# Optimization experiments

Hardware: AMD Instinct MI355X
Metric: run time of the kernel (lower is better)

Reference implementation:

```python
import jax, jax.numpy as jnp
import numpy as np

N = 32768
E = 262144
OUT = 512
H = 8
DH = OUT // H


def setup_inputs() -> dict:
    key = jax.random.key(0)
    ks = jax.random.split(key, 12)
    s = 0.02
    return {
        "h": jax.random.normal(ks[0], (N, 512), dtype=jnp.float32),
        "row": jax.random.randint(ks[1], (E,), 0, N, dtype=jnp.int32),
        "col": jax.random.randint(ks[2], (E,), 0, N, dtype=jnp.int32),
        "W_in": jax.random.normal(ks[3], (512, OUT), dtype=jnp.float32) * s,
        "b_in": jnp.zeros((OUT,), dtype=jnp.float32),
        "W_q": jax.random.normal(ks[4], (OUT, OUT), dtype=jnp.float32) * s,
        "b_q": jnp.zeros((OUT,), dtype=jnp.float32),
        "W_k": jax.random.normal(ks[5], (OUT, OUT), dtype=jnp.float32) * s,
        "b_k": jnp.zeros((OUT,), dtype=jnp.float32),
        "W_v": jax.random.normal(ks[6], (OUT, OUT), dtype=jnp.float32) * s,
        "b_v": jnp.zeros((OUT,), dtype=jnp.float32),
    }


def reference(h, row, col, W_in, b_in, W_q, b_q, W_k, b_k, W_v, b_v):
    scaling = DH ** -0.5
    x = h @ W_in + b_in                                   # [N, OUT]
    q = ((x @ W_q + b_q) * scaling).reshape(N, H, DH)     # [N, H, DH]
    k = (x @ W_k + b_k).reshape(N, H, DH)
    v = (x @ W_v + b_v).reshape(N, H, DH)

    # bsddmm: per-edge, per-head attention logits only at adjacency nonzeros
    logits = jnp.einsum("ehd,ehd->eh", q[row], k[col])    # [E, H]

    # sparse row-wise softmax over each node's incident edges
    m = jax.ops.segment_max(logits, row, num_segments=N)  # [N, H]
    ex = jnp.exp(logits - m[row])                         # [E, H]
    denom = jax.ops.segment_sum(ex, row, num_segments=N)  # [N, H]
    attn = ex / denom[row]                                # [E, H]

    # bspmm: aggregate v over neighbors with sparse attention weights
    out = jax.ops.segment_sum(attn[:, :, None] * v[col], row, num_segments=N)  # [N, H, DH]
    return out
```

## Files before the change

kernel.cpp:

```cpp
#include <hip/hip_runtime.h>

#define NN 32768
#define EE 262144
#define DM 512
#define NQKV 1536
#define NHEAD 8
#define DHEAD 64

typedef unsigned short u16;
typedef unsigned int u32;
typedef __attribute__((ext_vector_type(8))) short bf16x8;
typedef __attribute__((ext_vector_type(4))) float f32x4;
typedef __attribute__((ext_vector_type(8))) u16 u16x8;
typedef __attribute__((ext_vector_type(4))) u32 u32x4;

__device__ __forceinline__ float bf2f(u16 u) {
  union { u32 i; float f; } x; x.i = ((u32)u) << 16; return x.f;
}
__device__ __forceinline__ float bflo(u32 p) {
  union { u32 i; float f; } x; x.i = p << 16; return x.f;
}
__device__ __forceinline__ float bfhi(u32 p) {
  union { u32 i; float f; } x; x.i = p & 0xFFFF0000u; return x.f;
}
__device__ __forceinline__ u16 f2bf(float f) {
  union { float f; u32 i; } x; x.f = f;
  u32 r = x.i + 0x7FFFu + ((x.i >> 16) & 1u);
  return (u16)(r >> 16);
}

__device__ __forceinline__ void load_lds16(const u16* g, u16* l) {
  __builtin_amdgcn_global_load_lds(
      (const __attribute__((address_space(1))) char*)(const void*)g,
      (__attribute__((address_space(3))) char*)(void*)l, 16, 0, 0);
}

__device__ __forceinline__ int swz(int r, int s) {
  return s ^ (r & 3) ^ ((r >> 2) & 1);
}

#define GB_CASTH 8192
#define GB_CASTW 128
#define GB_CNTD  1024
#define GB_TCW   192
#define GB_BIAS  96
__global__ void prep_all(const float* __restrict__ h, u16* __restrict__ hb,
                         const float* __restrict__ Win, u16* __restrict__ Winb,
                         const int* __restrict__ row, int* __restrict__ deg,
                         const float* __restrict__ Wq, const float* __restrict__ Wk,
                         const float* __restrict__ Wv, u16* __restrict__ At,
                         const float* __restrict__ bin, const float* __restrict__ bq,
                         const float* __restrict__ bk, const float* __restrict__ bv,
                         float* __restrict__ bias) {
  __shared__ float t[64][65];
  const int tid = threadIdx.x;
  int b = blockIdx.x;

  if (b < GB_CASTH) {
    const int i = (b * 256 + tid) * 8;
    float4 a = *(const float4*)&h[i];
    float4 c = *(const float4*)&h[i + 4];
    u16x8 o = { f2bf(a.x), f2bf(a.y), f2bf(a.z), f2bf(a.w),
                f2bf(c.x), f2bf(c.y), f2bf(c.z), f2bf(c.w) };
    *(u16x8*)&hb[i] = o;
    return;
  }
  b -= GB_CASTH;
  if (b < GB_CASTW) {
    const int i = (b * 256 + tid) * 8;
    float4 a = *(const float4*)&Win[i];
    float4 c = *(const float4*)&Win[i + 4];
    u16x8 o = { f2bf(a.x), f2bf(a.y), f2bf(a.z), f2bf(a.w),
                f2bf(c.x), f2bf(c.y), f2bf(c.z), f2bf(c.w) };
    *(u16x8*)&Winb[i] = o;
    return;
  }
  b -= GB_CASTW;
  if (b < GB_CNTD) {
    const int e = b * 256 + tid;
    atomicAdd(&deg[row[e]], 1);
    return;
  }
  b -= GB_CNTD;
  if (b < GB_TCW) {
    const int z = b / 64;
    const int r64 = b % 64;
    const float* W = (z == 0) ? Wq : (z == 1) ? Wk : Wv;
    const float scale = (z == 0) ? 0.125f : 1.0f;
    const int m0 = (r64 >> 3) * 64;
    const int j0 = (r64 & 7) * 64;
    const int tx = tid & 63, ty = tid >> 6;
#pragma unroll
    for (int i = 0; i < 16; ++i) {
      const int r = ty * 16 + i;
      t[r][tx] = W[(size_t)(m0 + r) * 512 + (j0 + tx)];
    }
    __syncthreads();
#pragma unroll
    for (int i = 0; i < 16; ++i) {
      const int j = j0 + ty * 16 + i;
      const int pr = (z == 0) ? j : (512 + 2 * j + (z - 1));
      At[(size_t)pr * 512 + (m0 + tx)] = f2bf(t[tx][ty * 16 + i] * scale);
    }
    return;
  }
  b -= GB_TCW;
  {
    const int j = (b % 6) * 256 + tid;
    const int m0 = (b / 6) * 32;
    const float* Wsel; const float* bsel; int jj; float scale = 1.0f; int pos;
    if (j < 512)       { Wsel = Wq; bsel = bq; jj = j;        scale = 0.125f; pos = j; }
    else if (j < 1024) { Wsel = Wk; bsel = bk; jj = j - 512;  pos = 512 + 2 * jj; }
    else               { Wsel = Wv; bsel = bv; jj = j - 1024; pos = 513 + 2 * jj; }
    float s0 = 0.f, s1 = 0.f, s2 = 0.f, s3 = 0.f;
#pragma unroll
    for (int m = 0; m < 32; m += 4) {
      s0 = fmaf(bin[m0 + m],     Wsel[(size_t)(m0 + m)     * 512 + jj], s0);
      s1 = fmaf(bin[m0 + m + 1], Wsel[(size_t)(m0 + m + 1) * 512 + jj], s1);
      s2 = fmaf(bin[m0 + m + 2], Wsel[(size_t)(m0 + m + 2) * 512 + jj], s2);
      s3 = fmaf(bin[m0 + m + 3], Wsel[(size_t)(m0 + m + 3) * 512 + jj], s3);
    }
    float add = ((s0 + s1) + (s2 + s3)) * scale;
    if (m0 == 0) add += bsel[jj] * scale;
    atomicAdd(&bias[pos], add);
  }
}

__global__ void scan_deg(const int* __restrict__ deg, int* __restrict__ row_ptr,
                         int* __restrict__ cursor) {
  __shared__ int sums[1024];
  const int t = threadIdx.x;
  const int base = t * 32;
  int loc[32];
  int s = 0;
#pragma unroll
  for (int i = 0; i < 32; ++i) { loc[i] = s; s += deg[base + i]; }
  sums[t] = s;
  __syncthreads();
  for (int off = 1; off < 1024; off <<= 1) {
    int v = (t >= off) ? sums[t - off] : 0;
    __syncthreads();
    sums[t] += v;
    __syncthreads();
  }
  const int excl = sums[t] - s;
#pragma unroll
  for (int i = 0; i < 32; ++i) {
    const int val = excl + loc[i];
    row_ptr[base + i] = val;
    cursor[base + i] = val;
  }
  if (t == 1023) row_ptr[NN] = sums[1023];
}

__global__ void fill_csr(const int* __restrict__ row, const int* __restrict__ col,
                         int* __restrict__ cursor, int* __restrict__ dst) {
  const int e = blockIdx.x * 256 + threadIdx.x;
  const int r = row[e];
  const int p = atomicAdd(&cursor[r], 1);
  dst[p] = col[e];
}

__global__ __launch_bounds__(256, 2) void gemm_wt(
    const u16* __restrict__ A,
    const u16* __restrict__ B,
    u16* __restrict__ C) {
  __shared__ u16 As[2][128 * 32];
  __shared__ u16 Bs[2][128 * 32];
  const int tid = threadIdx.x;
  const int lane = tid & 63;
  const int wave = tid >> 6;
  const int quad = lane >> 4;
  const int l16 = lane & 15;
  const int m0 = blockIdx.y * 128;
  const int n0 = blockIdx.x * 128;
  const int wm = (wave >> 1) * 64;
  const int wn = (wave & 1) * 64;

  const int c0 = tid, c1 = tid + 256;
  const int r0 = c0 >> 2, ko0 = swz(r0, c0 & 3) * 8;
  const int r1 = c1 >> 2, ko1 = swz(r1, c1 & 3) * 8;
  const u16* Ag0 = A + (size_t)(m0 + r0) * DM + ko0;
  const u16* Ag1 = A + (size_t)(m0 + r1) * DM + ko1;
  const u16* Bg0 = B + (size_t)(n0 + r0) * DM + ko0;
  const u16* Bg1 = B + (size_t)(n0 + r1) * DM + ko1;

  f32x4 acc[4][4];
#pragma unroll
  for (int i = 0; i < 4; ++i)
#pragma unroll
    for (int j = 0; j < 4; ++j) acc[i][j] = (f32x4){0.f, 0.f, 0.f, 0.f};

  load_lds16(Ag0, &As[0][c0 * 8]);
  load_lds16(Bg0, &Bs[0][c0 * 8]);
  load_lds16(Ag1, &As[0][c1 * 8]);
  load_lds16(Bg1, &Bs[0][c1 * 8]);
  __syncthreads();

  int cur = 0;
#pragma unroll
  for (int kt = 32; kt < DM; kt += 32) {
    load_lds16(Ag0 + kt, &As[cur ^ 1][c0 * 8]);
    load_lds16(Bg0 + kt, &Bs[cur ^ 1][c0 * 8]);
    load_lds16(Ag1 + kt, &As[cur ^ 1][c1 * 8]);
    load_lds16(Bg1 + kt, &Bs[cur ^ 1][c1 * 8]);
    bf16x8 a[4], b[4];
#pragma unroll
    for (int i = 0; i < 4; ++i) {
      const int ra = wm + i * 16 + l16;
      const int rb = wn + i * 16 + l16;
      a[i] = *(const bf16x8*)&As[cur][ra * 32 + swz(ra, quad) * 8];
      b[i] = *(const bf16x8*)&Bs[cur][rb * 32 + swz(rb, quad) * 8];
    }
#pragma unroll
    for (int mi = 0; mi < 4; ++mi)
#pragma unroll
      for (int ni = 0; ni < 4; ++ni)
        acc[mi][ni] = __builtin_amdgcn_mfma_f32_16x16x32_bf16(a[mi], b[ni], acc[mi][ni], 0, 0, 0);
    __syncthreads();
    cur ^= 1;
  }
  {
    bf16x8 a[4], b[4];
#pragma unroll
    for (int i = 0; i < 4; ++i) {
      const int ra = wm + i * 16 + l16;
      const int rb = wn + i * 16 + l16;
      a[i] = *(const bf16x8*)&As[cur][ra * 32 + swz(ra, quad) * 8];
      b[i] = *(const bf16x8*)&Bs[cur][rb * 32 + swz(rb, quad) * 8];
    }
#pragma unroll
    for (int mi = 0; mi < 4; ++mi)
#pragma unroll
      for (int ni = 0; ni < 4; ++ni)
        acc[mi][ni] = __builtin_amdgcn_mfma_f32_16x16x32_bf16(a[mi], b[ni], acc[mi][ni], 0, 0, 0);
  }

#pragma unroll
  for (int ni = 0; ni < 4; ++ni) {
    const int coln = n0 + wn + ni * 16 + l16;
#pragma unroll
    for (int mi = 0; mi < 4; ++mi) {
#pragma unroll
      for (int r = 0; r < 4; ++r) {
        const int rowm = m0 + wm + mi * 16 + quad * 4 + r;
        C[(size_t)rowm * 512 + coln] = f2bf(acc[mi][ni][r]);
      }
    }
  }
}

__global__ __launch_bounds__(256, 2) void gemm_qkv(
    const u16* __restrict__ A,
    const u16* __restrict__ B,
    const float* __restrict__ bias,
    u16* __restrict__ C) {
  __shared__ u16 As[3][128 * 32];
  __shared__ u16 Bs[3][128 * 32];
  const int tid = threadIdx.x;
  const int lane = tid & 63;
  const int wave = tid >> 6;
  const int quad = lane >> 4;
  const int l16 = lane & 15;

  const int bid = blockIdx.y * 12 + blockIdx.x;
  const int sw = (bid & 7) * 384 + (bid >> 3);
  const int bx = sw % 12;
  const int by = sw / 12;
  const int m0 = by * 128;
  const int n0 = bx * 128;
  const int wm = (wave >> 1) * 64;
  const int wn = (wave & 1) * 64;

  const int c0 = tid, c1 = tid + 256;
  const int r0 = c0 >> 2, ko0 = swz(r0, c0 & 3) * 8;
  const int r1 = c1 >> 2, ko1 = swz(r1, c1 & 3) * 8;
  const u16* Ag0 = A + (size_t)(m0 + r0) * DM + ko0;
  const u16* Ag1 = A + (size_t)(m0 + r1) * DM + ko1;
  const u16* Bg0 = B + (size_t)(n0 + r0) * DM + ko0;
  const u16* Bg1 = B + (size_t)(n0 + r1) * DM + ko1;

  f32x4 acc[4][4];
#pragma unroll
  for (int i = 0; i < 4; ++i)
#pragma unroll
    for (int j = 0; j < 4; ++j) acc[i][j] = (f32x4){0.f, 0.f, 0.f, 0.f};

  load_lds16(Ag0, &As[0][c0 * 8]);
  load_lds16(Bg0, &Bs[0][c0 * 8]);
  load_lds16(Ag1, &As[0][c1 * 8]);
  load_lds16(Bg1, &Bs[0][c1 * 8]);
  load_lds16(Ag0 + 32, &As[1][c0 * 8]);
  load_lds16(Bg0 + 32, &Bs[1][c0 * 8]);
  load_lds16(Ag1 + 32, &As[1][c1 * 8]);
  load_lds16(Bg1 + 32, &Bs[1][c1 * 8]);

#pragma unroll
  for (int t = 0; t < 16; ++t) {
    const int bt = t % 3;
    if (t < 15) asm volatile("s_waitcnt vmcnt(4) lgkmcnt(0)\n\ts_barrier" ::: "memory");
    else        asm volatile("s_waitcnt vmcnt(0) lgkmcnt(0)\n\ts_barrier" ::: "memory");
    if (t < 14) {
      const int b2 = (t + 2) % 3;
      const int kg = (t + 2) * 32;
      load_lds16(Ag0 + kg, &As[b2][c0 * 8]);
      load_lds16(Bg0 + kg, &Bs[b2][c0 * 8]);
      load_lds16(Ag1 + kg, &As[b2][c1 * 8]);
      load_lds16(Bg1 + kg, &Bs[b2][c1 * 8]);
    }
    bf16x8 a[4], b[4];
#pragma unroll
    for (int i = 0; i < 4; ++i) {
      const int ra = wm + i * 16 + l16;
      const int rb = wn + i * 16 + l16;
      a[i] = *(const bf16x8*)&As[bt][ra * 32 + swz(ra, quad) * 8];
      b[i] = *(const bf16x8*)&Bs[bt][rb * 32 + swz(rb, quad) * 8];
    }
#pragma unroll
    for (int mi = 0; mi < 4; ++mi)
#pragma unroll
      for (int ni = 0; ni < 4; ++ni)
        acc[mi][ni] = __builtin_amdgcn_mfma_f32_16x16x32_bf16(a[mi], b[ni], acc[mi][ni], 0, 0, 0);
  }

#pragma unroll
  for (int ni = 0; ni < 4; ++ni) {
    const int coln = n0 + wn + ni * 16 + l16;
    const float bv = bias[coln];
#pragma unroll
    for (int mi = 0; mi < 4; ++mi) {
#pragma unroll
      for (int r = 0; r < 4; ++r) {
        const int rowm = m0 + wm + mi * 16 + quad * 4 + r;
        C[(size_t)rowm * NQKV + coln] = f2bf(acc[mi][ni][r] + bv);
      }
    }
  }
}

__global__ __launch_bounds__(256) void attn_agg(
    const u16* __restrict__ qkv16, const u32* __restrict__ qkv32,
    const int* __restrict__ row_ptr, const int* __restrict__ dst,
    float* __restrict__ out) {
  const int gt = blockIdx.x * 256 + threadIdx.x;
  const int node = gt >> 6;
  const int lane = gt & 63;
  const u16x8 qr = *(const u16x8*)&qkv16[(size_t)node * NQKV + lane * 8];
  float qf[8];
#pragma unroll
  for (int j = 0; j < 8; ++j) qf[j] = bf2f(qr[j]);

  const int beg = row_ptr[node];
  const int end = row_ptr[node + 1];
  float acc[8] = {0.f,0.f,0.f,0.f,0.f,0.f,0.f,0.f};
  float denom = 0.f;

  for (int e = beg; e < end; e += 4) {
    u32 p[4][8];
    int idx[4];
#pragma unroll
    for (int jj = 0; jj < 4; ++jj) {
      const int ee = min(e + jj, end - 1);
      idx[jj] = dst[ee];
    }
#pragma unroll
    for (int jj = 0; jj < 4; ++jj) {
      const u32* pp = qkv32 + (size_t)idx[jj] * 768 + 256 + lane * 8;
      *(u32x4*)&p[jj][0] = *(const u32x4*)pp;
      *(u32x4*)&p[jj][4] = *(const u32x4*)(pp + 4);
    }
#pragma unroll
    for (int jj = 0; jj < 4; ++jj) {
      float s = 0.f;
#pragma unroll
      for (int j = 0; j < 8; ++j) s = fmaf(qf[j], bflo(p[jj][j]), s);
      s += __shfl_xor(s, 1, 64);
      s += __shfl_xor(s, 2, 64);
      s += __shfl_xor(s, 4, 64);
      const float ex = (e + jj < end) ? __expf(s) : 0.f;
      denom += ex;
#pragma unroll
      for (int j = 0; j < 8; ++j) acc[j] = fmaf(ex, bfhi(p[jj][j]), acc[j]);
    }
  }

  const float inv = (end > beg) ? (1.0f / denom) : 0.f;
  float4 o0 = { acc[0] * inv, acc[1] * inv, acc[2] * inv, acc[3] * inv };
  float4 o1 = { acc[4] * inv, acc[5] * inv, acc[6] * inv, acc[7] * inv };
  float* op = &out[(size_t)node * 512 + lane * 8];
  *(float4*)op = o0;
  *(float4*)(op + 4) = o1;
}

extern "C" void kernel_launch(void* const* d_in, const int* in_sizes, int n_in,
                              void* d_out, int out_size, void* d_ws, size_t ws_size,
                              hipStream_t stream) {
  const float* h   = (const float*)d_in[0];
  const int*   row = (const int*)d_in[1];
  const int*   col = (const int*)d_in[2];
  const float* Win = (const float*)d_in[3];
  const float* bin = (const float*)d_in[4];
  const float* Wq  = (const float*)d_in[5];
  const float* bq  = (const float*)d_in[6];
  const float* Wk  = (const float*)d_in[7];
  const float* bk  = (const float*)d_in[8];
  const float* Wv  = (const float*)d_in[9];
  const float* bv  = (const float*)d_in[10];
  float* out = (float*)d_out;

  char* ws = (char*)d_ws;
  u16*   qkv     = (u16*)(ws + 0);
  u16*   hb      = (u16*)(ws + 100663296);
  u16*   Wt      = (u16*)(ws + 134217728);
  float* bias    = (float*)(ws + 135790592);
  int*   deg     = (int*)(ws + 135796736);
  int*   row_ptr = (int*)(ws + 135927808);
  int*   cursor  = (int*)(ws + 136058888);
  int*   dst     = (int*)(ws + 136189960);
  u16*   At      = (u16*)(ws + 0);
  u16*   Winb    = (u16*)(ws + 1572864);

  (void)hipMemsetAsync(deg, 0, NN * sizeof(int), stream);
  (void)hipMemsetAsync(bias, 0, NQKV * sizeof(float), stream);
  hipLaunchKernelGGL(prep_all,
                     dim3(GB_CASTH + GB_CASTW + GB_CNTD + GB_TCW + GB_BIAS),
                     dim3(256), 0, stream,
                     h, hb, Win, Winb, row, deg, Wq, Wk, Wv, At,
                     bin, bq, bk, bv, bias);
  hipLaunchKernelGGL(scan_deg,  dim3(1), dim3(1024), 0, stream, deg, row_ptr, cursor);
  hipLaunchKernelGGL(fill_csr,  dim3(EE / 256), dim3(256), 0, stream, row, col, cursor, dst);
  hipLaunchKernelGGL(gemm_wt,   dim3(512 / 128, 1536 / 128), dim3(256), 0, stream, At, Winb, Wt);
  hipLaunchKernelGGL(gemm_qkv,  dim3(NQKV / 128, NN / 128), dim3(256), 0, stream, hb, Wt, bias, qkv);
  hipLaunchKernelGGL(attn_agg,  dim3((NN * 64) / 256), dim3(256), 0, stream,
                     qkv, (const u32*)qkv, row_ptr, dst, out);
}
```

Measured before the change: 338.8 us.

## Fold weight-product GEMM into prep kernel using fp32 SIMT tiles

Removes the separate transposed-weight cast and bf16 MFMA gemm_wt launch. The prep kernel now directly computes the combined (W_q|W_k|W_v)^T·W_in^T product in fp32 with shared-memory tiled FMAs, placing these long blocks first in the grid. Bias folding now uses one block per column group over all 512 rows with no atomics, which also drops the bias memset. This saves one kernel launch plus the intermediate casts, but does the 1536x512x512 weight product on SIMT lanes instead of matrix cores, so those 192 blocks may become a long tail.

```diff
diff --git a/kernel.cpp b/kernel.cpp
--- a/kernel.cpp
+++ b/kernel.cpp
@@ -39,90 +39,101 @@
   return s ^ (r & 3) ^ ((r >> 2) & 1);
 }
 
+#define GB_WT    192
+#define GB_BIAS  6
+#define GB_CNTD  1024
 #define GB_CASTH 8192
-#define GB_CASTW 128
-#define GB_CNTD  1024
-#define GB_TCW   192
-#define GB_BIAS  96
-__global__ void prep_all(const float* __restrict__ h, u16* __restrict__ hb,
-                         const float* __restrict__ Win, u16* __restrict__ Winb,
-                         const int* __restrict__ row, int* __restrict__ deg,
-                         const float* __restrict__ Wq, const float* __restrict__ Wk,
-                         const float* __restrict__ Wv, u16* __restrict__ At,
-                         const float* __restrict__ bin, const float* __restrict__ bq,
-                         const float* __restrict__ bk, const float* __restrict__ bv,
-                         float* __restrict__ bias) {
-  __shared__ float t[64][65];
+__global__ __launch_bounds__(256) void prep_mega(
+    const float* __restrict__ h, u16* __restrict__ hb,
+    const float* __restrict__ Win,
+    const float* __restrict__ Wq, const float* __restrict__ Wk,
+    const float* __restrict__ Wv, u16* __restrict__ Wt,
+    const float* __restrict__ bin, const float* __restrict__ bq,
+    const float* __restrict__ bk, const float* __restrict__ bv,
+    float* __restrict__ bias,
+    const int* __restrict__ row, int* __restrict__ deg) {
+  __shared__ float As[32][68];
+  __shared__ float Bs[64][36];
   const int tid = threadIdx.x;
   int b = blockIdx.x;
 
-  if (b < GB_CASTH) {
+  if (b < GB_WT) {
+    const int jt = b >> 3;
+    const int kt = b & 7;
+    const int z = jt >> 3;
+    const float* W = (z == 0) ? Wq : (z == 1) ? Wk : Wv;
+    const float scale = (z == 0) ? 0.125f : 1.0f;
+    const int jj0 = (jt & 7) * 64;
+    const int kk0 = kt * 64;
+    const int tj = tid >> 4, tk = tid & 15;
+    float acc[4][4] = {};
+    for (int k0 = 0; k0 < 512; k0 += 32) {
+#pragma unroll
+      for (int i = 0; i < 8; ++i) {
+        const int idx = tid + i * 256;
+        const int ami = idx >> 6, ajo = idx & 63;
+        As[ami][ajo] = W[(size_t)(k0 + ami) * 512 + jj0 + ajo];
+        const int bkk = idx >> 5, bmi = idx & 31;
+        Bs[bkk][bmi] = Win[(size_t)(kk0 + bkk) * 512 + k0 + bmi];
+      }
+      __syncthreads();
+#pragma unroll
+      for (int mi = 0; mi < 32; ++mi) {
+        float4 av = *(const float4*)&As[mi][tj * 4];
+        const float* ap = (const float*)&av;
+        float bv4[4] = { Bs[tk * 4 + 0][mi], Bs[tk * 4 + 1][mi],
+                         Bs[tk * 4 + 2][mi], Bs[tk * 4 + 3][mi] };
+#pragma unroll
+        for (int a2 = 0; a2 < 4; ++a2)
+#pragma unroll
+          for (int b2 = 0; b2 < 4; ++b2)
+            acc[a2][b2] = fmaf(ap[a2], bv4[b2], acc[a2][b2]);
+      }
+      __syncthreads();
+    }
+#pragma unroll
+    for (int a2 = 0; a2 < 4; ++a2) {
+      const int j = jt * 64 + tj * 4 + a2;
+      const int pr = (j < 512) ? j
+                   : (j < 1024) ? (512 + 2 * (j - 512))
+                                : (513 + 2 * (j - 1024));
+#pragma unroll
+      for (int b2 = 0; b2 < 4; ++b2)
+        Wt[(size_t)pr * 512 + kk0 + tk * 4 + b2] = f2bf(acc[a2][b2] * scale);
+    }
+    return;
+  }
+  b -= GB_WT;
+  if (b < GB_BIAS) {
+    const int j = b * 256 + tid;
+    const float* Wsel; const float* bsel; int jj; float scale = 1.0f; int pos;
+    if (j < 512)       { Wsel = Wq; bsel = bq; jj = j;        scale = 0.125f; pos = j; }
+    else if (j < 1024) { Wsel = Wk; bsel = bk; jj = j - 512;  pos = 512 + 2 * jj; }
+    else               { Wsel = Wv; bsel = bv; jj = j - 1024; pos = 513 + 2 * jj; }
+    float s0 = 0.f, s1 = 0.f, s2 = 0.f, s3 = 0.f;
+    for (int m = 0; m < 512; m += 4) {
+      s0 = fmaf(bin[m],     Wsel[(size_t)m * 512 + jj],       s0);
+      s1 = fmaf(bin[m + 1], Wsel[(size_t)(m + 1) * 512 + jj], s1);
+      s2 = fmaf(bin[m + 2], Wsel[(size_t)(m + 2) * 512 + jj], s2);
+      s3 = fmaf(bin[m + 3], Wsel[(size_t)(m + 3) * 512 + jj], s3);
+    }
+    bias[pos] = (((s0 + s1) + (s2 + s3)) + bsel[jj]) * scale;
+    return;
+  }
+  b -= GB_BIAS;
+  if (b < GB_CNTD) {
+    const int e = b * 256 + tid;
+    atomicAdd(&deg[row[e]], 1);
+    return;
+  }
+  b -= GB_CNTD;
+  {
     const int i = (b * 256 + tid) * 8;
     float4 a = *(const float4*)&h[i];
     float4 c = *(const float4*)&h[i + 4];
     u16x8 o = { f2bf(a.x), f2bf(a.y), f2bf(a.z), f2bf(a.w),
                 f2bf(c.x), f2bf(c.y), f2bf(c.z), f2bf(c.w) };
     *(u16x8*)&hb[i] = o;
-    return;
-  }
-  b -= GB_CASTH;
-  if (b < GB_CASTW) {
-    const int i = (b * 256 + tid) * 8;
-    float4 a = *(const float4*)&Win[i];
-    float4 c = *(const float4*)&Win[i + 4];
-    u16x8 o = { f2bf(a.x), f2bf(a.y), f2bf(a.z), f2bf(a.w),
-                f2bf(c.x), f2bf(c.y), f2bf(c.z), f2bf(c.w) };
-    *(u16x8*)&Winb[i] = o;
-    return;
-  }
-  b -= GB_CASTW;
-  if (b < GB_CNTD) {
-    const int e = b * 256 + tid;
-    atomicAdd(&deg[row[e]], 1);
-    return;
-  }
-  b -= GB_CNTD;
-  if (b < GB_TCW) {
-    const int z = b / 64;
-    const int r64 = b % 64;
-    const float* W = (z == 0) ? Wq : (z == 1) ? Wk : Wv;
-    const float scale = (z == 0) ? 0.125f : 1.0f;
-    const int m0 = (r64 >> 3) * 64;
-    const int j0 = (r64 & 7) * 64;
-    const int tx = tid & 63, ty = tid >> 6;
-#pragma unroll
-    for (int i = 0; i < 16; ++i) {
-      const int r = ty * 16 + i;
-      t[r][tx] = W[(size_t)(m0 + r) * 512 + (j0 + tx)];
-    }
-    __syncthreads();
-#pragma unroll
-    for (int i = 0; i < 16; ++i) {
-      const int j = j0 + ty * 16 + i;
-      const int pr = (z == 0) ? j : (512 + 2 * j + (z - 1));
-      At[(size_t)pr * 512 + (m0 + tx)] = f2bf(t[tx][ty * 16 + i] * scale);
-    }
-    return;
-  }
-  b -= GB_TCW;
-  {
-    const int j = (b % 6) * 256 + tid;
-    const int m0 = (b / 6) * 32;
-    const float* Wsel; const float* bsel; int jj; float scale = 1.0f; int pos;
-    if (j < 512)       { Wsel = Wq; bsel = bq; jj = j;        scale = 0.125f; pos = j; }
-    else if (j < 1024) { Wsel = Wk; bsel = bk; jj = j - 512;  pos = 512 + 2 * jj; }
-    else               { Wsel = Wv; bsel = bv; jj = j - 1024; pos = 513 + 2 * jj; }
-    float s0 = 0.f, s1 = 0.f, s2 = 0.f, s3 = 0.f;
-#pragma unroll
-    for (int m = 0; m < 32; m += 4) {
-      s0 = fmaf(bin[m0 + m],     Wsel[(size_t)(m0 + m)     * 512 + jj], s0);
-      s1 = fmaf(bin[m0 + m + 1], Wsel[(size_t)(m0 + m + 1) * 512 + jj], s1);
-      s2 = fmaf(bin[m0 + m + 2], Wsel[(size_t)(m0 + m + 2) * 512 + jj], s2);
-      s3 = fmaf(bin[m0 + m + 3], Wsel[(size_t)(m0 + m + 3) * 512 + jj], s3);
-    }
-    float add = ((s0 + s1) + (s2 + s3)) * scale;
-    if (m0 == 0) add += bsel[jj] * scale;
-    atomicAdd(&bias[pos], add);
   }
 }
 
@@ -159,95 +170,6 @@
   const int r = row[e];
   const int p = atomicAdd(&cursor[r], 1);
   dst[p] = col[e];
-}
-
-__global__ __launch_bounds__(256, 2) void gemm_wt(
-    const u16* __restrict__ A,
-    const u16* __restrict__ B,
-    u16* __restrict__ C) {
-  __shared__ u16 As[2][128 * 32];
-  __shared__ u16 Bs[2][128 * 32];
-  const int tid = threadIdx.x;
-  const int lane = tid & 63;
-  const int wave = tid >> 6;
-  const int quad = lane >> 4;
-  const int l16 = lane & 15;
-  const int m0 = blockIdx.y * 128;
-  const int n0 = blockIdx.x * 128;
-  const int wm = (wave >> 1) * 64;
-  const int wn = (wave & 1) * 64;
-
-  const int c0 = tid, c1 = tid + 256;
-  const int r0 = c0 >> 2, ko0 = swz(r0, c0 & 3) * 8;
-  const int r1 = c1 >> 2, ko1 = swz(r1, c1 & 3) * 8;
-  const u16* Ag0 = A + (size_t)(m0 + r0) * DM + ko0;
-  const u16* Ag1 = A + (size_t)(m0 + r1) * DM + ko1;
-  const u16* Bg0 = B + (size_t)(n0 + r0) * DM + ko0;
-  const u16* Bg1 = B + (size_t)(n0 + r1) * DM + ko1;
-
-  f32x4 acc[4][4];
-#pragma unroll
-  for (int i = 0; i < 4; ++i)
-#pragma unroll
-    for (int j = 0; j < 4; ++j) acc[i][j] = (f32x4){0.f, 0.f, 0.f, 0.f};
-
-  load_lds16(Ag0, &As[0][c0 * 8]);
-  load_lds16(Bg0, &Bs[0][c0 * 8]);
-  load_lds16(Ag1, &As[0][c1 * 8]);
-  load_lds16(Bg1, &Bs[0][c1 * 8]);
-  __syncthreads();
-
-  int cur = 0;
-#pragma unroll
-  for (int kt = 32; kt < DM; kt += 32) {
-    load_lds16(Ag0 + kt, &As[cur ^ 1][c0 * 8]);
-    load_lds16(Bg0 + kt, &Bs[cur ^ 1][c0 * 8]);
-    load_lds16(Ag1 + kt, &As[cur ^ 1][c1 * 8]);
-    load_lds16(Bg1 + kt, &Bs[cur ^ 1][c1 * 8]);
-    bf16x8 a[4], b[4];
-#pragma unroll
-    for (int i = 0; i < 4; ++i) {
-      const int ra = wm + i * 16 + l16;
-      const int rb = wn + i * 16 + l16;
-      a[i] = *(const bf16x8*)&As[cur][ra * 32 + swz(ra, quad) * 8];
-      b[i] = *(const bf16x8*)&Bs[cur][rb * 32 + swz(rb, quad) * 8];
-    }
-#pragma unroll
-    for (int mi = 0; mi < 4; ++mi)
-#pragma unroll
-      for (int ni = 0; ni < 4; ++ni)
-        acc[mi][ni] = __builtin_amdgcn_mfma_f32_16x16x32_bf16(a[mi], b[ni], acc[mi][ni], 0, 0, 0);
-    __syncthreads();
-    cur ^= 1;
-  }
-  {
-    bf16x8 a[4], b[4];
-#pragma unroll
-    for (int i = 0; i < 4; ++i) {
-      const int ra = wm + i * 16 + l16;
-      const int rb = wn + i * 16 + l16;
-      a[i] = *(const bf16x8*)&As[cur][ra * 32 + swz(ra, quad) * 8];
-      b[i] = *(const bf16x8*)&Bs[cur][rb * 32 + swz(rb, quad) * 8];
-    }
-#pragma unroll
-    for (int mi = 0; mi < 4; ++mi)
-#pragma unroll
-      for (int ni = 0; ni < 4; ++ni)
-        acc[mi][ni] = __builtin_amdgcn_mfma_f32_16x16x32_bf16(a[mi], b[ni], acc[mi][ni], 0, 0, 0);
-  }
-
-#pragma unroll
-  for (int ni = 0; ni < 4; ++ni) {
-    const int coln = n0 + wn + ni * 16 + l16;
-#pragma unroll
-    for (int mi = 0; mi < 4; ++mi) {
-#pragma unroll
-      for (int r = 0; r < 4; ++r) {
-        const int rowm = m0 + wm + mi * 16 + quad * 4 + r;
-        C[(size_t)rowm * 512 + coln] = f2bf(acc[mi][ni][r]);
-      }
-    }
-  }
 }
 
 __global__ __launch_bounds__(256, 2) void gemm_qkv(
@@ -417,19 +339,13 @@
   int*   row_ptr = (int*)(ws + 135927808);
   int*   cursor  = (int*)(ws + 136058888);
   int*   dst     = (int*)(ws + 136189960);
-  u16*   At      = (u16*)(ws + 0);
-  u16*   Winb    = (u16*)(ws + 1572864);
 
   (void)hipMemsetAsync(deg, 0, NN * sizeof(int), stream);
-  (void)hipMemsetAsync(bias, 0, NQKV * sizeof(float), stream);
-  hipLaunchKernelGGL(prep_all,
-                     dim3(GB_CASTH + GB_CASTW + GB_CNTD + GB_TCW + GB_BIAS),
-                     dim3(256), 0, stream,
-                     h, hb, Win, Winb, row, deg, Wq, Wk, Wv, At,
-                     bin, bq, bk, bv, bias);
+  hipLaunchKernelGGL(prep_mega,
+                     dim3(GB_WT + GB_BIAS + GB_CNTD + GB_CASTH), dim3(256), 0, stream,
+                     h, hb, Win, Wq, Wk, Wv, Wt, bin, bq, bk, bv, bias, row, deg);
   hipLaunchKernelGGL(scan_deg,  dim3(1), dim3(1024), 0, stream, deg, row_ptr, cursor);
   hipLaunchKernelGGL(fill_csr,  dim3(EE / 256), dim3(256), 0, stream, row, col, cursor, dst);
-  hipLaunchKernelGGL(gemm_wt,   dim3(512 / 128, 1536 / 128), dim3(256), 0, stream, At, Winb, Wt);
   hipLaunchKernelGGL(gemm_qkv,  dim3(NQKV / 128, NN / 128), dim3(256), 0, stream, hb, Wt, bias, qkv);
   hipLaunchKernelGGL(attn_agg,  dim3((NN * 64) / 256), dim3(256), 0, stream,
                      qkv, (const u32*)qkv, row_ptr, dst, out);
```

New measurement: 361.8 us. +6.8%, slower.

## Enlarge QKV GEMM to 256x256 tiles with 8 waves and LDS-staged stores

Applied to the files above, without the earlier changes.

Rewrites the fused QKV projection GEMM to use 256x256 output tiles per 512-thread block with K-steps of 64. Global-to-LDS loads are double-buffered in half-tiles interleaved with MFMA slabs, and MFMA sections run under raised wave priority. The aim is to cut global and LDS traffic per FLOP and raise arithmetic intensity. The epilogue now stages results through swizzled LDS to emit coalesced 16-byte stores. In exchange it uses 128KB of LDS and one block per CU, which lowers occupancy and latency hiding.

```diff
diff --git a/kernel.cpp b/kernel.cpp
--- a/kernel.cpp
+++ b/kernel.cpp
@@ -250,92 +250,118 @@
   }
 }
 
-__global__ __launch_bounds__(256, 2) void gemm_qkv(
+__global__ __launch_bounds__(512, 1) void gemm_qkv(
     const u16* __restrict__ A,
     const u16* __restrict__ B,
     const float* __restrict__ bias,
     u16* __restrict__ C) {
-  __shared__ u16 As[3][128 * 32];
-  __shared__ u16 Bs[3][128 * 32];
+  __shared__ __align__(16) u16 lds[65536];
   const int tid = threadIdx.x;
   const int lane = tid & 63;
   const int wave = tid >> 6;
   const int quad = lane >> 4;
   const int l16 = lane & 15;
 
-  const int bid = blockIdx.y * 12 + blockIdx.x;
-  const int sw = (bid & 7) * 384 + (bid >> 3);
-  const int bx = sw % 12;
-  const int by = sw / 12;
-  const int m0 = by * 128;
-  const int n0 = bx * 128;
-  const int wm = (wave >> 1) * 64;
-  const int wn = (wave & 1) * 64;
-
-  const int c0 = tid, c1 = tid + 256;
-  const int r0 = c0 >> 2, ko0 = swz(r0, c0 & 3) * 8;
-  const int r1 = c1 >> 2, ko1 = swz(r1, c1 & 3) * 8;
-  const u16* Ag0 = A + (size_t)(m0 + r0) * DM + ko0;
-  const u16* Ag1 = A + (size_t)(m0 + r1) * DM + ko1;
-  const u16* Bg0 = B + (size_t)(n0 + r0) * DM + ko0;
-  const u16* Bg1 = B + (size_t)(n0 + r1) * DM + ko1;
-
-  f32x4 acc[4][4];
-#pragma unroll
-  for (int i = 0; i < 4; ++i)
-#pragma unroll
-    for (int j = 0; j < 4; ++j) acc[i][j] = (f32x4){0.f, 0.f, 0.f, 0.f};
-
-  load_lds16(Ag0, &As[0][c0 * 8]);
-  load_lds16(Bg0, &Bs[0][c0 * 8]);
-  load_lds16(Ag1, &As[0][c1 * 8]);
-  load_lds16(Bg1, &Bs[0][c1 * 8]);
-  load_lds16(Ag0 + 32, &As[1][c0 * 8]);
-  load_lds16(Bg0 + 32, &Bs[1][c0 * 8]);
-  load_lds16(Ag1 + 32, &As[1][c1 * 8]);
-  load_lds16(Bg1 + 32, &Bs[1][c1 * 8]);
-
-#pragma unroll
-  for (int t = 0; t < 16; ++t) {
-    const int bt = t % 3;
-    if (t < 15) asm volatile("s_waitcnt vmcnt(4) lgkmcnt(0)\n\ts_barrier" ::: "memory");
-    else        asm volatile("s_waitcnt vmcnt(0) lgkmcnt(0)\n\ts_barrier" ::: "memory");
-    if (t < 14) {
-      const int b2 = (t + 2) % 3;
-      const int kg = (t + 2) * 32;
-      load_lds16(Ag0 + kg, &As[b2][c0 * 8]);
-      load_lds16(Bg0 + kg, &Bs[b2][c0 * 8]);
-      load_lds16(Ag1 + kg, &As[b2][c1 * 8]);
-      load_lds16(Bg1 + kg, &Bs[b2][c1 * 8]);
-    }
-    bf16x8 a[4], b[4];
-#pragma unroll
-    for (int i = 0; i < 4; ++i) {
-      const int ra = wm + i * 16 + l16;
-      const int rb = wn + i * 16 + l16;
-      a[i] = *(const bf16x8*)&As[bt][ra * 32 + swz(ra, quad) * 8];
-      b[i] = *(const bf16x8*)&Bs[bt][rb * 32 + swz(rb, quad) * 8];
-    }
-#pragma unroll
-    for (int mi = 0; mi < 4; ++mi)
-#pragma unroll
-      for (int ni = 0; ni < 4; ++ni)
-        acc[mi][ni] = __builtin_amdgcn_mfma_f32_16x16x32_bf16(a[mi], b[ni], acc[mi][ni], 0, 0, 0);
-  }
-
-#pragma unroll
-  for (int ni = 0; ni < 4; ++ni) {
-    const int coln = n0 + wn + ni * 16 + l16;
-    const float bv = bias[coln];
-#pragma unroll
-    for (int mi = 0; mi < 4; ++mi) {
-#pragma unroll
-      for (int r = 0; r < 4; ++r) {
-        const int rowm = m0 + wm + mi * 16 + quad * 4 + r;
-        C[(size_t)rowm * NQKV + coln] = f2bf(acc[mi][ni][r] + bv);
+  const int bid = blockIdx.y * 6 + blockIdx.x;
+  const int sw = (bid & 7) * 96 + (bid >> 3);
+  const int bx = sw % 6, by = sw / 6;
+  const int m0 = by * 256, n0 = bx * 256;
+
+  const int r0 = tid >> 3;
+  const int sc = (tid & 7) ^ (r0 & 7);
+  const u16* Ag = A + (size_t)(m0 + r0) * DM + sc * 8;
+  const u16* Bg = B + (size_t)(n0 + r0) * DM + sc * 8;
+  const int ls0 = tid * 8, ls1 = ls0 + 4096;
+
+#define AOFF(d, hh) (((d) * 2 + (hh)) * 8192)
+#define BOFF(d, hh) (32768 + ((d) * 2 + (hh)) * 8192)
+#define STAGE_A(t, hh) do { \
+    load_lds16(Ag + (size_t)(hh) * 128 * DM + (t) * 64,            &lds[AOFF((t) & 1, (hh)) + ls0]); \
+    load_lds16(Ag + (size_t)(hh) * 128 * DM + 64 * DM + (t) * 64,  &lds[AOFF((t) & 1, (hh)) + ls1]); } while (0)
+#define STAGE_B(t, hh) do { \
+    load_lds16(Bg + (size_t)(hh) * 128 * DM + (t) * 64,            &lds[BOFF((t) & 1, (hh)) + ls0]); \
+    load_lds16(Bg + (size_t)(hh) * 128 * DM + 64 * DM + (t) * 64,  &lds[BOFF((t) & 1, (hh)) + ls1]); } while (0)
+
+  const int cx0 = ((quad ^ (l16 & 7)) * 8) + l16 * 64;
+  const int cx1 = (((quad + 4) ^ (l16 & 7)) * 8) + l16 * 64;
+
+  f32x4 acc[4][4][2];
+#pragma unroll
+  for (int p = 0; p < 4; ++p)
+#pragma unroll
+    for (int i = 0; i < 4; ++i)
+#pragma unroll
+      for (int j = 0; j < 2; ++j) acc[p][i][j] = (f32x4){0.f, 0.f, 0.f, 0.f};
+
+#define SLAB(t, p) do { \
+    const int _d = (t) & 1; \
+    const int _ab = AOFF(_d, (p) >> 1) + ((p) & 1) * 4096; \
+    const int _bk = (wave + (p)) & 7; \
+    const int _bb = BOFF(_d, _bk >> 2) + (_bk & 3) * 2048; \
+    bf16x8 a0[4], a1[4], b0[2], b1[2]; \
+    _Pragma("unroll") for (int i = 0; i < 4; ++i) { \
+      a0[i] = *(const bf16x8*)&lds[_ab + i * 1024 + cx0]; \
+      a1[i] = *(const bf16x8*)&lds[_ab + i * 1024 + cx1]; } \
+    _Pragma("unroll") for (int j = 0; j < 2; ++j) { \
+      b0[j] = *(const bf16x8*)&lds[_bb + j * 1024 + cx0]; \
+      b1[j] = *(const bf16x8*)&lds[_bb + j * 1024 + cx1]; } \
+    __builtin_amdgcn_s_setprio(1); \
+    _Pragma("unroll") for (int i = 0; i < 4; ++i) \
+      _Pragma("unroll") for (int j = 0; j < 2; ++j) \
+        acc[p][i][j] = __builtin_amdgcn_mfma_f32_16x16x32_bf16(a0[i], b0[j], acc[p][i][j], 0, 0, 0); \
+    _Pragma("unroll") for (int i = 0; i < 4; ++i) \
+      _Pragma("unroll") for (int j = 0; j < 2; ++j) \
+        acc[p][i][j] = __builtin_amdgcn_mfma_f32_16x16x32_bf16(a1[i], b1[j], acc[p][i][j], 0, 0, 0); \
+    __builtin_amdgcn_s_setprio(0); } while (0)
+
+  STAGE_B(0, 0); STAGE_B(0, 1); STAGE_A(0, 0); STAGE_A(0, 1);
+
+#pragma unroll
+  for (int t = 0; t < 8; ++t) {
+    asm volatile("s_waitcnt vmcnt(2) lgkmcnt(0)\ns_barrier" ::: "memory");
+    if (t < 7) { STAGE_B(t + 1, 0); STAGE_B(t + 1, 1); }
+    SLAB(t, 0);
+    if (t < 7) { STAGE_A(t + 1, 0); }
+    SLAB(t, 1);
+    if (t < 7) asm volatile("s_waitcnt vmcnt(6) lgkmcnt(0)\ns_barrier" ::: "memory");
+    else       asm volatile("s_waitcnt vmcnt(0) lgkmcnt(0)\ns_barrier" ::: "memory");
+    if (t < 7) { STAGE_A(t + 1, 1); }
+    SLAB(t, 2);
+    SLAB(t, 3);
+  }
+
+  asm volatile("s_waitcnt lgkmcnt(0)\ns_barrier" ::: "memory");
+#pragma unroll
+  for (int p = 0; p < 4; ++p) {
+    const int bblk = (wave + p) & 7;
+#pragma unroll
+    for (int j = 0; j < 2; ++j) {
+      const int col = bblk * 32 + j * 16 + l16;
+      const float bv = bias[n0 + col];
+#pragma unroll
+      for (int i = 0; i < 4; ++i) {
+#pragma unroll
+        for (int r = 0; r < 4; ++r) {
+          const int rr = p * 64 + i * 16 + quad * 4 + r;
+          lds[rr * 256 + (col ^ (((rr >> 2) & 7) << 3))] = f2bf(acc[p][i][j][r] + bv);
+        }
       }
     }
   }
+  __syncthreads();
+#pragma unroll
+  for (int k = 0; k < 16; ++k) {
+    const int idx = k * 512 + tid;
+    const int rr = idx >> 5;
+    const int cc = (idx & 31) * 8;
+    *(u16x8*)&C[(size_t)(m0 + rr) * NQKV + n0 + cc] =
+        *(const u16x8*)&lds[rr * 256 + (cc ^ (((rr >> 2) & 7) << 3))];
+  }
+#undef SLAB
+#undef STAGE_A
+#undef STAGE_B
+#undef AOFF
+#undef BOFF
 }
 
 __global__ __launch_bounds__(256) void attn_agg(
@@ -430,7 +456,7 @@
   hipLaunchKernelGGL(scan_deg,  dim3(1), dim3(1024), 0, stream, deg, row_ptr, cursor);
   hipLaunchKernelGGL(fill_csr,  dim3(EE / 256), dim3(256), 0, stream, row, col, cursor, dst);
   hipLaunchKernelGGL(gemm_wt,   dim3(512 / 128, 1536 / 128), dim3(256), 0, stream, At, Winb, Wt);
-  hipLaunchKernelGGL(gemm_qkv,  dim3(NQKV / 128, NN / 128), dim3(256), 0, stream, hb, Wt, bias, qkv);
+  hipLaunchKernelGGL(gemm_qkv,  dim3(NQKV / 256, NN / 256), dim3(512), 0, stream, hb, Wt, bias, qkv);
   hipLaunchKernelGGL(attn_agg,  dim3((NN * 64) / 256), dim3(256), 0, stream,
                      qkv, (const u32*)qkv, row_ptr, dst, out);
 }
```

Measured after the change: 334.7 us. Within noise of the previous version (-1.2%).
